# Performance work log

Measured on AMD Instinct MI355X. Metric: run time of the kernel, lower is better.

## Reference

```python
import jax, jax.numpy as jnp
import numpy as np

N, D_IN, D_OUT = 16384, 1024, 1024
E, R, TOP_K = 8, 16, 2
ALPHA = 32.0
SCALING = ALPHA / R  # standard LoRA scaling alpha/rank


def setup_inputs() -> dict:
    key = jax.random.key(0)
    k_tok, k_wb, k_a, k_b, k_g = jax.random.split(key, 5)
    tokens = jax.random.normal(k_tok, (N, D_IN), dtype=jnp.float32)
    # frozen attention projection
    W_base = jax.random.normal(k_wb, (D_IN, D_OUT), dtype=jnp.float32) * (1.0 / np.sqrt(D_IN))
    # per-expert LoRA factors
    A = jax.random.normal(k_a, (E, D_IN, R), dtype=jnp.float32) * 0.02
    B = jax.random.normal(k_b, (E, R, D_OUT), dtype=jnp.float32) * 0.02
    # router
    W_gate = jax.random.normal(k_g, (D_IN, E), dtype=jnp.float32) * (1.0 / np.sqrt(D_IN))
    return {"tokens": tokens, "W_base": W_base, "A": A, "B": B, "W_gate": W_gate}


def reference(tokens, W_base, A, B, W_gate):
    # Router: top-k gating with softmax over the selected logits
    router_logits = tokens @ W_gate                      # [N, E]
    topk_vals, selected_experts = jax.lax.top_k(router_logits, TOP_K)  # [N, K]
    expert_weights = jax.nn.softmax(topk_vals, axis=-1)  # [N, K]

    # Dense combine weights: zeros except selected experts
    gates = jnp.zeros((tokens.shape[0], E), dtype=tokens.dtype)
    gates = gates.at[jnp.arange(tokens.shape[0])[:, None], selected_experts].set(expert_weights)  # [N, E]

    # Frozen base projection
    base_out = tokens @ W_base                           # [N, D_out]

    # LoRA experts: low-rank intermediate [N, E, R] is small (rank 16)
    h = jnp.einsum('nd,edr->ner', tokens, A)             # [N, E, R]
    h = h * gates[:, :, None]                            # gate before expanding to D_out
    lora_out = jnp.einsum('ner,erm->nm', h, B)           # [N, D_out]

    out = base_out + SCALING * lora_out
    return out, router_logits, selected_experts, expert_weights
```

## Files before the change

### kernel.cpp

```cpp
#include <hip/hip_runtime.h>
#include <hip/hip_bf16.h>
#include <cstdint>
#include <cfloat>

#define NTOK 16384
#define DIN  1024
#define DOUT 1024
#define NEXP 8
#define RLORA 16
#define KTOT 1152
#define SCALE_LORA 2.0f

typedef __attribute__((ext_vector_type(8))) short bf16x8;
typedef __attribute__((ext_vector_type(4))) float f32x4;

__device__ __forceinline__ unsigned short f2bf(float f) {
  __hip_bfloat16 h = __float2bfloat16(f);
  unsigned short u;
  __builtin_memcpy(&u, &h, 2);
  return u;
}

__device__ __forceinline__ void gld_lds16(const void* g, void* l) {
  __builtin_amdgcn_global_load_lds((const __attribute__((address_space(1))) void*)g,
                                   (__attribute__((address_space(3))) void*)l,
                                   16, 0, 0);
}

__global__ __launch_bounds__(256) void k_prep(const float* __restrict__ Wb,
                                              const float* __restrict__ B,
                                              const float* __restrict__ A,
                                              const float* __restrict__ Wg,
                                              unsigned short* __restrict__ WcatT,
                                              unsigned short* __restrict__ AcatT,
                                              float* __restrict__ WgT) {
  __shared__ unsigned short Tbuf[256 * 17];
  const int bid = blockIdx.x;
  const int t = threadIdx.x;
  if (bid < 288) {
    unsigned short (*T)[66] = (unsigned short (*)[66])Tbuf;
    const int k0 = (bid % 18) * 64, j0 = (bid / 18) * 64;
#pragma unroll
    for (int p = 0; p < 4; ++p) {
      int kk = p * 16 + (t >> 4);
      int c4 = (t & 15) * 4;
      int k = k0 + kk;
      const float* src = (k < 1024) ? (Wb + (size_t)k * 1024) : (B + (size_t)(k - 1024) * 1024);
      float4 v = *(const float4*)(src + j0 + c4);
      T[kk][c4 + 0] = f2bf(v.x); T[kk][c4 + 1] = f2bf(v.y);
      T[kk][c4 + 2] = f2bf(v.z); T[kk][c4 + 3] = f2bf(v.w);
    }
    __syncthreads();
#pragma unroll
    for (int p = 0; p < 2; ++p) {
      int jj = p * 32 + (t >> 3);
      int kc = (t & 7) * 8;
      unsigned short buf[8];
#pragma unroll
      for (int i = 0; i < 8; ++i) buf[i] = T[kc + i][jj];
      uint4 u; __builtin_memcpy(&u, buf, 16);
      *(uint4*)(WcatT + (size_t)(j0 + jj) * KTOT + k0 + kc) = u;
    }
  } else if (bid < 320) {
    unsigned short (*T)[17] = (unsigned short (*)[17])Tbuf;
    const int e = (bid - 288) >> 2, d0 = ((bid - 288) & 3) * 256;
#pragma unroll
    for (int p = 0; p < 4; ++p) {
      int idx = p * 256 + t;
      int d = idx >> 2;
      int rr = (idx & 3) * 4;
      float4 v = *(const float4*)(A + (size_t)e * 16384 + (size_t)(d0 + d) * 16 + rr);
      T[d][rr + 0] = f2bf(v.x); T[d][rr + 1] = f2bf(v.y);
      T[d][rr + 2] = f2bf(v.z); T[d][rr + 3] = f2bf(v.w);
    }
    __syncthreads();
#pragma unroll
    for (int p = 0; p < 2; ++p) {
      int slot = p * 256 + t;
      int r = slot >> 5;
      int dc = (slot & 31) * 8;
      unsigned short buf[8];
#pragma unroll
      for (int i = 0; i < 8; ++i) buf[i] = T[dc + i][r];
      uint4 u; __builtin_memcpy(&u, buf, 16);
      *(uint4*)(AcatT + (size_t)(e * 16 + r) * 1024 + d0 + dc) = u;
    }
  } else {
    int d = (bid - 320) * 256 + t;
    float4 a = *(const float4*)(Wg + (size_t)d * 8);
    float4 b = *(const float4*)(Wg + (size_t)d * 8 + 4);
    WgT[0 * 1024 + d] = a.x; WgT[1 * 1024 + d] = a.y;
    WgT[2 * 1024 + d] = a.z; WgT[3 * 1024 + d] = a.w;
    WgT[4 * 1024 + d] = b.x; WgT[5 * 1024 + d] = b.y;
    WgT[6 * 1024 + d] = b.z; WgT[7 * 1024 + d] = b.w;
  }
}

__global__ __launch_bounds__(256) void k_router(const float* __restrict__ tokens,
                                                const float* __restrict__ WgT,
                                                float* __restrict__ out_logits,
                                                float* __restrict__ out_sel,
                                                float* __restrict__ out_w,
                                                unsigned short* __restrict__ Xcat,
                                                float4* __restrict__ gateinfo) {
  const int wid = threadIdx.x >> 6;
  const int lane = threadIdx.x & 63;
  const int t0 = (blockIdx.x * 4 + wid) * 2;

  float4 xa[4], xb[4];
  const float* x0 = tokens + (size_t)t0 * DIN;
  const float* x1 = x0 + DIN;
#pragma unroll
  for (int j = 0; j < 4; ++j) {
    xa[j] = *(const float4*)(x0 + j * 256 + lane * 4);
    xb[j] = *(const float4*)(x1 + j * 256 + lane * 4);
  }

#pragma unroll
  for (int tt = 0; tt < 2; ++tt) {
    unsigned short* xbp = Xcat + (size_t)(t0 + tt) * KTOT;
    const float4* xv = tt ? xb : xa;
#pragma unroll
    for (int j = 0; j < 4; ++j) {
      const float* xf = (const float*)&xv[j];
      unsigned short hb[4];
#pragma unroll
      for (int m = 0; m < 4; ++m) hb[m] = f2bf(xf[m]);
      uint2 u;
      __builtin_memcpy(&u, hb, 8);
      *(uint2*)(xbp + j * 256 + lane * 4) = u;
    }
  }

  float accA[8] = {0,0,0,0,0,0,0,0}, accB[8] = {0,0,0,0,0,0,0,0};
#pragma unroll
  for (int j = 0; j < 4; ++j) {
#pragma unroll
    for (int e = 0; e < 8; ++e) {
      float4 wv = *(const float4*)(WgT + (size_t)e * 1024 + j * 256 + lane * 4);
      accA[e] = fmaf(xa[j].x, wv.x, fmaf(xa[j].y, wv.y,
                fmaf(xa[j].z, wv.z, fmaf(xa[j].w, wv.w, accA[e]))));
      accB[e] = fmaf(xb[j].x, wv.x, fmaf(xb[j].y, wv.y,
                fmaf(xb[j].z, wv.z, fmaf(xb[j].w, wv.w, accB[e]))));
    }
  }
#pragma unroll
  for (int s = 1; s < 64; s <<= 1) {
#pragma unroll
    for (int e = 0; e < 8; ++e) {
      accA[e] += __shfl_xor(accA[e], s, 64);
      accB[e] += __shfl_xor(accB[e], s, 64);
    }
  }

#pragma unroll
  for (int tt = 0; tt < 2; ++tt) {
    const float* acc = tt ? accB : accA;
    int t = t0 + tt;
    float v0 = -FLT_MAX, v1 = -FLT_MAX;
    int i0 = -1, i1 = -1;
#pragma unroll
    for (int e = 0; e < 8; ++e) {
      float v = acc[e];
      if (v > v0) { v1 = v0; i1 = i0; v0 = v; i0 = e; }
      else if (v > v1) { v1 = v; i1 = e; }
    }
    float ex = expf(v1 - v0);
    float inv = 1.0f / (1.0f + ex);
    float w0 = inv, w1 = ex * inv;
    if (lane == 0) {
      float4* lg = (float4*)(out_logits + (size_t)t * 8);
      lg[0] = make_float4(acc[0], acc[1], acc[2], acc[3]);
      lg[1] = make_float4(acc[4], acc[5], acc[6], acc[7]);
      *(float2*)(out_sel + (size_t)t * 2) = make_float2((float)i0, (float)i1);
      *(float2*)(out_w + (size_t)t * 2) = make_float2(w0, w1);
      gateinfo[t] = make_float4((float)i0, (float)i1, w0 * SCALE_LORA, w1 * SCALE_LORA);
    }
  }
}

__global__ __launch_bounds__(256) void k_hgemm(const unsigned short* __restrict__ Xg,
                                               const unsigned short* __restrict__ Ag,
                                               const float4* __restrict__ gateinfo,
                                               unsigned short* __restrict__ Xout) {
  constexpr int BK = 64;
  __shared__ alignas(16) unsigned short As[64 * BK];
  __shared__ alignas(16) unsigned short Bs[64 * BK];
  const int tid = threadIdx.x;
  const int lane = tid & 63;
  const int wid = tid >> 6;
  const int id = blockIdx.x;
  const int xcd = id & 7, s5 = id >> 3;
  const int n0 = (s5 & 1) * 64;
  const int m0 = (xcd * 32 + (s5 >> 1)) * 64;
  const int wm = (wid >> 1) * 32, wn = (wid & 1) * 32;
  const int quad = lane >> 4, r16 = lane & 15;

  f32x4 acc[2][2] = {};

  for (int k0 = 0; k0 < 1024; k0 += BK) {
#pragma unroll
    for (int i = 0; i < 2; ++i) {
      int s = i * 256 + tid;
      int r = s >> 3, c = s & 7;
      int q = c ^ ((r >> 1) & 7);
      gld_lds16(Xg + (size_t)(m0 + r) * KTOT + k0 + q * 8, (char*)As + s * 16);
    }
#pragma unroll
    for (int i = 0; i < 2; ++i) {
      int s = i * 256 + tid;
      int r = s >> 3, c = s & 7;
      int q = c ^ ((r >> 1) & 7);
      gld_lds16(Ag + (size_t)(n0 + r) * 1024 + k0 + q * 8, (char*)Bs + s * 16);
    }
    __syncthreads();

#pragma unroll
    for (int h = 0; h < 2; ++h) {
      bf16x8 af[2], bfr[2];
#pragma unroll
      for (int mi = 0; mi < 2; ++mi) {
        int m = wm + mi * 16 + r16;
        int slot = m * 8 + ((h * 4 + quad) ^ ((m >> 1) & 7));
        af[mi] = *(const bf16x8*)((const char*)As + slot * 16);
      }
#pragma unroll
      for (int ni = 0; ni < 2; ++ni) {
        int n = wn + ni * 16 + r16;
        int slot = n * 8 + ((h * 4 + quad) ^ ((n >> 1) & 7));
        bfr[ni] = *(const bf16x8*)((const char*)Bs + slot * 16);
      }
#pragma unroll
      for (int mi = 0; mi < 2; ++mi)
#pragma unroll
        for (int ni = 0; ni < 2; ++ni)
          acc[mi][ni] = __builtin_amdgcn_mfma_f32_16x16x32_bf16(af[mi], bfr[ni], acc[mi][ni], 0, 0, 0);
    }
    __syncthreads();
  }

#pragma unroll
  for (int mi = 0; mi < 2; ++mi)
#pragma unroll
    for (int r = 0; r < 4; ++r) {
      int row = m0 + wm + mi * 16 + quad * 4 + r;
      float4 gi = gateinfo[row];
      int ie0 = (int)gi.x, ie1 = (int)gi.y;
#pragma unroll
      for (int ni = 0; ni < 2; ++ni) {
        int c = n0 + wn + ni * 16 + r16;
        int e = c >> 4;
        float h = acc[mi][ni][r];
        float v = (e == ie0) ? gi.z * h : ((e == ie1) ? gi.w * h : 0.f);
        Xout[(size_t)row * KTOT + 1024 + c] = f2bf(v);
      }
    }
}

__global__ __launch_bounds__(512, 2) void k_gemm_main(const unsigned short* __restrict__ Xg,
                                                      const unsigned short* __restrict__ Wgm,
                                                      float* __restrict__ C) {
  __shared__ alignas(16) unsigned short As[2][2][128 * 64];
  __shared__ alignas(16) unsigned short Bs[2][2][128 * 64];
  const int tid = threadIdx.x;
  const int lane = tid & 63;
  const int wid = tid >> 6;
  const int id = blockIdx.x;
  const int xcd = id & 7, loc = id >> 3;
  const int gid = xcd * 32 + loc;
  const int m0 = (gid >> 2) * 256;
  const int n0 = (gid & 3) * 256;
  const int wr64 = (wid >> 2) * 64;
  const int wc32 = (wid & 3) * 32;
  const int quad = lane >> 4, r16 = lane & 15;

  f32x4 acc[2][2][4][2] = {};
  bf16x8 af[4][2];
  bf16x8 bf_a[2][2];
  bf16x8 bf_b[2][2];

#define STAGE_A(SL, HF, KT)                                                   \
  {                                                                           \
    _Pragma("unroll")                                                         \
    for (int i_ = 0; i_ < 2; ++i_) {                                          \
      int s_ = i_ * 512 + tid;                                                \
      int r_ = s_ >> 3, c_ = s_ & 7;                                          \
      int q_ = c_ ^ ((r_ >> 1) & 7);                                          \
      gld_lds16(Xg + (size_t)(m0 + (HF) * 128 + r_) * KTOT + (KT) * 64 + q_ * 8, \
                (char*)As[SL][HF] + s_ * 16);                                 \
    }                                                                         \
  }
#define STAGE_B(SL, HF, KT)                                                   \
  {                                                                           \
    _Pragma("unroll")                                                         \
    for (int i_ = 0; i_ < 2; ++i_) {                                          \
      int s_ = i_ * 512 + tid;                                                \
      int r_ = s_ >> 3, c_ = s_ & 7;                                          \
      int q_ = c_ ^ ((r_ >> 1) & 7);                                          \
      gld_lds16(Wgm + (size_t)(n0 + (HF) * 128 + r_) * KTOT + (KT) * 64 + q_ * 8, \
                (char*)Bs[SL][HF] + s_ * 16);                                 \
    }                                                                         \
  }
#define DS_A(SL, HF)                                                          \
  {                                                                           \
    _Pragma("unroll")                                                         \
    for (int mi_ = 0; mi_ < 4; ++mi_) {                                       \
      int rh_ = wr64 + mi_ * 16 + r16;                                        \
      int sw_ = (rh_ >> 1) & 7;                                               \
      af[mi_][0] = *(const bf16x8*)((const char*)As[SL][HF] +                 \
                                    (rh_ * 8 + (quad ^ sw_)) * 16);           \
      af[mi_][1] = *(const bf16x8*)((const char*)As[SL][HF] +                 \
                                    (rh_ * 8 + ((4 + quad) ^ sw_)) * 16);     \
    }                                                                         \
  }
#define DS_B(DEST, SL, HF)                                                    \
  {                                                                           \
    _Pragma("unroll")                                                         \
    for (int ni_ = 0; ni_ < 2; ++ni_) {                                       \
      int rh_ = wc32 + ni_ * 16 + r16;                                        \
      int sw_ = (rh_ >> 1) & 7;                                               \
      DEST[ni_][0] = *(const bf16x8*)((const char*)Bs[SL][HF] +               \
                                      (rh_ * 8 + (quad ^ sw_)) * 16);         \
      DEST[ni_][1] = *(const bf16x8*)((const char*)Bs[SL][HF] +               \
                                      (rh_ * 8 + ((4 + quad) ^ sw_)) * 16);   \
    }                                                                         \
  }
#define VM(N) asm volatile("s_waitcnt vmcnt(" #N ")" ::: "memory")

#define PH(TOP, WIN, MH, NH, BF)                                              \
  {                                                                           \
    TOP;                                                                      \
    asm volatile("" ::: "memory");                                            \
    __builtin_amdgcn_s_barrier();                                             \
    asm volatile("s_waitcnt lgkmcnt(0)" ::: "memory");                        \
    __builtin_amdgcn_sched_barrier(0);                                        \
    WIN;                                                                      \
    __builtin_amdgcn_sched_barrier(0);                                        \
    __builtin_amdgcn_s_setprio(1);                                            \
    _Pragma("unroll")                                                         \
    for (int kk_ = 0; kk_ < 2; ++kk_)                                         \
      _Pragma("unroll")                                                       \
      for (int mi_ = 0; mi_ < 4; ++mi_)                                       \
        _Pragma("unroll")                                                     \
        for (int ni_ = 0; ni_ < 2; ++ni_)                                     \
          acc[MH][NH][mi_][ni_] = __builtin_amdgcn_mfma_f32_16x16x32_bf16(    \
              af[mi_][kk_], BF[ni_][kk_], acc[MH][NH][mi_][ni_], 0, 0, 0);    \
    __builtin_amdgcn_s_setprio(0);                                            \
    asm volatile("" ::: "memory");                                            \
    __builtin_amdgcn_s_barrier();                                             \
  }

  STAGE_A(0, 0, 0); STAGE_B(0, 0, 0); STAGE_B(0, 1, 0); STAGE_A(0, 1, 0);
  VM(2);
  __builtin_amdgcn_s_barrier();
  DS_B(bf_a, 0, 0);

  for (int it = 0; it < 9; ++it) {
    const int kt1 = 2 * it + 1;
    const int kt2 = (2 * it + 2 < 18) ? 2 * it + 2 : 17;
    PH(DS_A(0, 0); STAGE_A(1, 0, kt1); STAGE_B(1, 0, kt1),
       DS_B(bf_b, 0, 1), 0, 0, bf_a)
    PH(STAGE_B(1, 1, kt1); VM(6), , 0, 1, bf_b)
    PH(DS_A(0, 1), , 1, 1, bf_b)
    PH(STAGE_A(1, 1, kt1); VM(2), DS_B(bf_b, 1, 0), 1, 0, bf_a)
    PH(DS_A(1, 0); STAGE_A(0, 0, kt2); STAGE_B(0, 0, kt2),
       DS_B(bf_a, 1, 1), 0, 0, bf_b)
    PH(STAGE_B(0, 1, kt2); VM(6), , 0, 1, bf_a)
    PH(DS_A(1, 1), , 1, 1, bf_a)
    PH(STAGE_A(0, 1, kt2); VM(2), DS_B(bf_a, 0, 0), 1, 0, bf_b)
  }
  asm volatile("s_waitcnt vmcnt(0) lgkmcnt(0)" ::: "memory");
#undef PH
#undef VM
#undef DS_B
#undef DS_A
#undef STAGE_B
#undef STAGE_A

#pragma unroll
  for (int mh = 0; mh < 2; ++mh)
#pragma unroll
    for (int nh = 0; nh < 2; ++nh)
#pragma unroll
      for (int mi = 0; mi < 4; ++mi)
#pragma unroll
        for (int ni = 0; ni < 2; ++ni)
#pragma unroll
          for (int r = 0; r < 4; ++r) {
            int row = m0 + mh * 128 + wr64 + mi * 16 + quad * 4 + r;
            int cc = n0 + nh * 128 + wc32 + ni * 16 + r16;
            C[(size_t)row * 1024 + cc] = acc[mh][nh][mi][ni][r];
          }
}

extern "C" void kernel_launch(void* const* d_in, const int* in_sizes, int n_in,
                              void* d_out, int out_size, void* d_ws, size_t ws_size,
                              hipStream_t stream) {
  const float* tokens = (const float*)d_in[0];
  const float* Wb     = (const float*)d_in[1];
  const float* A      = (const float*)d_in[2];
  const float* B      = (const float*)d_in[3];
  const float* Wg     = (const float*)d_in[4];
  float* out = (float*)d_out;

  char* ws = (char*)d_ws;
  unsigned short* Xcat  = (unsigned short*)(ws);
  unsigned short* WcatT = (unsigned short*)(ws + 37748736);
  unsigned short* AcatT = (unsigned short*)(ws + 40108032);
  float4*         ginfo = (float4*)(ws + 40370176);
  float*          WgT   = (float*)(ws + 40632320);

  float* out_logits = out + (size_t)16384 * 1024;
  float* out_sel    = out_logits + (size_t)16384 * 8;
  float* out_w      = out_sel + (size_t)16384 * 2;

  k_prep<<<dim3(324), dim3(256), 0, stream>>>(Wb, B, A, Wg, WcatT, AcatT, WgT);
  k_router<<<dim3(2048), dim3(256), 0, stream>>>(tokens, WgT, out_logits, out_sel, out_w, Xcat, ginfo);
  k_hgemm<<<dim3(512), dim3(256), 0, stream>>>(Xcat, AcatT, ginfo, Xcat);
  k_gemm_main<<<dim3(256), dim3(512), 0, stream>>>(Xcat, WcatT, out);
}
```

Before: 190.0 us.

## Double-buffer LoRA h-GEMM with BK=128 and widen router bf16 stores

The LoRA intermediate GEMM now uses K tiles of 128 held in two LDS buffers, so the next tile's global-to-LDS loads are issued before the MFMAs on the current tile. One barrier per iteration replaces the previous load-sync-compute-sync pattern. The router kernel now loads 8 contiguous floats per lane and writes 16-byte bf16 stores instead of 8-byte ones. The trade-off is higher LDS use per block (64 KB), which may reduce occupancy. The h-GEMM is a small share of the total work next to the main base GEMM.

```diff
diff --git a/kernel.cpp b/kernel.cpp
--- a/kernel.cpp
+++ b/kernel.cpp
@@ -107,43 +107,47 @@
   const int lane = threadIdx.x & 63;
   const int t0 = (blockIdx.x * 4 + wid) * 2;
 
-  float4 xa[4], xb[4];
+  float4 xa[2][2], xb[2][2];
   const float* x0 = tokens + (size_t)t0 * DIN;
   const float* x1 = x0 + DIN;
 #pragma unroll
-  for (int j = 0; j < 4; ++j) {
-    xa[j] = *(const float4*)(x0 + j * 256 + lane * 4);
-    xb[j] = *(const float4*)(x1 + j * 256 + lane * 4);
-  }
+  for (int j = 0; j < 2; ++j)
+#pragma unroll
+    for (int h = 0; h < 2; ++h) {
+      xa[j][h] = *(const float4*)(x0 + j * 512 + lane * 8 + h * 4);
+      xb[j][h] = *(const float4*)(x1 + j * 512 + lane * 8 + h * 4);
+    }
 
 #pragma unroll
   for (int tt = 0; tt < 2; ++tt) {
     unsigned short* xbp = Xcat + (size_t)(t0 + tt) * KTOT;
-    const float4* xv = tt ? xb : xa;
-#pragma unroll
-    for (int j = 0; j < 4; ++j) {
-      const float* xf = (const float*)&xv[j];
-      unsigned short hb[4];
-#pragma unroll
-      for (int m = 0; m < 4; ++m) hb[m] = f2bf(xf[m]);
-      uint2 u;
-      __builtin_memcpy(&u, hb, 8);
-      *(uint2*)(xbp + j * 256 + lane * 4) = u;
+#pragma unroll
+    for (int j = 0; j < 2; ++j) {
+      const float* xf = tt ? (const float*)&xb[j][0] : (const float*)&xa[j][0];
+      unsigned short hb[8];
+#pragma unroll
+      for (int m = 0; m < 8; ++m) hb[m] = f2bf(xf[m]);
+      uint4 u;
+      __builtin_memcpy(&u, hb, 16);
+      *(uint4*)(xbp + j * 512 + lane * 8) = u;
     }
   }
 
   float accA[8] = {0,0,0,0,0,0,0,0}, accB[8] = {0,0,0,0,0,0,0,0};
 #pragma unroll
-  for (int j = 0; j < 4; ++j) {
-#pragma unroll
-    for (int e = 0; e < 8; ++e) {
-      float4 wv = *(const float4*)(WgT + (size_t)e * 1024 + j * 256 + lane * 4);
-      accA[e] = fmaf(xa[j].x, wv.x, fmaf(xa[j].y, wv.y,
-                fmaf(xa[j].z, wv.z, fmaf(xa[j].w, wv.w, accA[e]))));
-      accB[e] = fmaf(xb[j].x, wv.x, fmaf(xb[j].y, wv.y,
-                fmaf(xb[j].z, wv.z, fmaf(xb[j].w, wv.w, accB[e]))));
-    }
-  }
+  for (int j = 0; j < 2; ++j)
+#pragma unroll
+    for (int e = 0; e < 8; ++e)
+#pragma unroll
+      for (int h = 0; h < 2; ++h) {
+        float4 wv = *(const float4*)(WgT + (size_t)e * 1024 + j * 512 + lane * 8 + h * 4);
+        const float4& a4 = xa[j][h];
+        const float4& b4 = xb[j][h];
+        accA[e] = fmaf(a4.x, wv.x, fmaf(a4.y, wv.y,
+                  fmaf(a4.z, wv.z, fmaf(a4.w, wv.w, accA[e]))));
+        accB[e] = fmaf(b4.x, wv.x, fmaf(b4.y, wv.y,
+                  fmaf(b4.z, wv.z, fmaf(b4.w, wv.w, accB[e]))));
+      }
 #pragma unroll
   for (int s = 1; s < 64; s <<= 1) {
 #pragma unroll
@@ -183,9 +187,9 @@
                                                const unsigned short* __restrict__ Ag,
                                                const float4* __restrict__ gateinfo,
                                                unsigned short* __restrict__ Xout) {
-  constexpr int BK = 64;
-  __shared__ alignas(16) unsigned short As[64 * BK];
-  __shared__ alignas(16) unsigned short Bs[64 * BK];
+  constexpr int BK = 128;
+  __shared__ alignas(16) unsigned short As[2][64 * BK];
+  __shared__ alignas(16) unsigned short Bs[2][64 * BK];
   const int tid = threadIdx.x;
   const int lane = tid & 63;
   const int wid = tid >> 6;
@@ -198,46 +202,66 @@
 
   f32x4 acc[2][2] = {};
 
-  for (int k0 = 0; k0 < 1024; k0 += BK) {
-#pragma unroll
-    for (int i = 0; i < 2; ++i) {
-      int s = i * 256 + tid;
-      int r = s >> 3, c = s & 7;
-      int q = c ^ ((r >> 1) & 7);
-      gld_lds16(Xg + (size_t)(m0 + r) * KTOT + k0 + q * 8, (char*)As + s * 16);
-    }
-#pragma unroll
-    for (int i = 0; i < 2; ++i) {
-      int s = i * 256 + tid;
-      int r = s >> 3, c = s & 7;
-      int q = c ^ ((r >> 1) & 7);
-      gld_lds16(Ag + (size_t)(n0 + r) * 1024 + k0 + q * 8, (char*)Bs + s * 16);
-    }
-    __syncthreads();
-
-#pragma unroll
-    for (int h = 0; h < 2; ++h) {
-      bf16x8 af[2], bfr[2];
-#pragma unroll
-      for (int mi = 0; mi < 2; ++mi) {
-        int m = wm + mi * 16 + r16;
-        int slot = m * 8 + ((h * 4 + quad) ^ ((m >> 1) & 7));
-        af[mi] = *(const bf16x8*)((const char*)As + slot * 16);
-      }
-#pragma unroll
-      for (int ni = 0; ni < 2; ++ni) {
-        int n = wn + ni * 16 + r16;
-        int slot = n * 8 + ((h * 4 + quad) ^ ((n >> 1) & 7));
-        bfr[ni] = *(const bf16x8*)((const char*)Bs + slot * 16);
-      }
+#define HSTAGE(d, k0s)                                                        \
+  {                                                                           \
+    _Pragma("unroll")                                                         \
+    for (int i_ = 0; i_ < 4; ++i_) {                                          \
+      int s_ = i_ * 256 + tid;                                                \
+      int r_ = s_ >> 4, c_ = s_ & 15;                                         \
+      int q_ = c_ ^ ((r_ >> 1) & 7);                                          \
+      gld_lds16(Xg + (size_t)(m0 + r_) * KTOT + (k0s) + q_ * 8,               \
+                (char*)As[d] + s_ * 16);                                      \
+    }                                                                         \
+    _Pragma("unroll")                                                         \
+    for (int i_ = 0; i_ < 4; ++i_) {                                          \
+      int s_ = i_ * 256 + tid;                                                \
+      int r_ = s_ >> 4, c_ = s_ & 15;                                         \
+      int q_ = c_ ^ ((r_ >> 1) & 7);                                          \
+      gld_lds16(Ag + (size_t)(n0 + r_) * 1024 + (k0s) + q_ * 8,               \
+                (char*)Bs[d] + s_ * 16);                                      \
+    }                                                                         \
+  }
+
+  HSTAGE(0, 0);
+  asm volatile("s_waitcnt vmcnt(0)" ::: "memory");
+  __builtin_amdgcn_s_barrier();
+
+  int cur = 0;
+  for (int t = 0; t < 8; ++t) {
+    if (t < 7) HSTAGE(cur ^ 1, (t + 1) * BK);
+
+    bf16x8 af[2][4], bfr[2][4];
+#pragma unroll
+    for (int mi = 0; mi < 2; ++mi) {
+      int m = wm + mi * 16 + r16;
+      int sw = (m >> 1) & 7;
+#pragma unroll
+      for (int h = 0; h < 4; ++h)
+        af[mi][h] = *(const bf16x8*)((const char*)As[cur] +
+                                     (m * 16 + ((h * 4 + quad) ^ sw)) * 16);
+    }
+#pragma unroll
+    for (int ni = 0; ni < 2; ++ni) {
+      int n = wn + ni * 16 + r16;
+      int sw = (n >> 1) & 7;
+#pragma unroll
+      for (int h = 0; h < 4; ++h)
+        bfr[ni][h] = *(const bf16x8*)((const char*)Bs[cur] +
+                                      (n * 16 + ((h * 4 + quad) ^ sw)) * 16);
+    }
+#pragma unroll
+    for (int h = 0; h < 4; ++h)
 #pragma unroll
       for (int mi = 0; mi < 2; ++mi)
 #pragma unroll
         for (int ni = 0; ni < 2; ++ni)
-          acc[mi][ni] = __builtin_amdgcn_mfma_f32_16x16x32_bf16(af[mi], bfr[ni], acc[mi][ni], 0, 0, 0);
-    }
-    __syncthreads();
-  }
+          acc[mi][ni] = __builtin_amdgcn_mfma_f32_16x16x32_bf16(af[mi][h], bfr[ni][h], acc[mi][ni], 0, 0, 0);
+
+    asm volatile("s_waitcnt vmcnt(0)" ::: "memory");
+    __builtin_amdgcn_s_barrier();
+    cur ^= 1;
+  }
+#undef HSTAGE
 
 #pragma unroll
   for (int mi = 0; mi < 2; ++mi)
```

Result: slower. 194.6 us (+2.4%).

## Fuse router and LoRA down-projection into one kernel with LDS-resident token tile

Applied to the files above, without the earlier changes.

Merges the router kernel and the low-rank h-GEMM into a single kernel. Each block converts 32 token rows to bf16, keeps them in swizzled shared memory and computes gating, then runs the rank GEMM against double-buffered A tiles without re-reading X from global memory. Gate info stays in shared memory instead of a global buffer. The cost is 64KB+ of LDS per block, which lowers occupancy, and only 512 blocks that each process 32 rows serially in the router phase.

```diff
diff --git a/kernel.cpp b/kernel.cpp
--- a/kernel.cpp
+++ b/kernel.cpp
@@ -96,164 +96,157 @@
   }
 }
 
-__global__ __launch_bounds__(256) void k_router(const float* __restrict__ tokens,
-                                                const float* __restrict__ WgT,
-                                                float* __restrict__ out_logits,
-                                                float* __restrict__ out_sel,
-                                                float* __restrict__ out_w,
-                                                unsigned short* __restrict__ Xcat,
-                                                float4* __restrict__ gateinfo) {
-  const int wid = threadIdx.x >> 6;
-  const int lane = threadIdx.x & 63;
-  const int t0 = (blockIdx.x * 4 + wid) * 2;
-
-  float4 xa[4], xb[4];
-  const float* x0 = tokens + (size_t)t0 * DIN;
-  const float* x1 = x0 + DIN;
-#pragma unroll
-  for (int j = 0; j < 4; ++j) {
-    xa[j] = *(const float4*)(x0 + j * 256 + lane * 4);
-    xb[j] = *(const float4*)(x1 + j * 256 + lane * 4);
-  }
-
-#pragma unroll
-  for (int tt = 0; tt < 2; ++tt) {
-    unsigned short* xbp = Xcat + (size_t)(t0 + tt) * KTOT;
-    const float4* xv = tt ? xb : xa;
-#pragma unroll
-    for (int j = 0; j < 4; ++j) {
-      const float* xf = (const float*)&xv[j];
-      unsigned short hb[4];
-#pragma unroll
-      for (int m = 0; m < 4; ++m) hb[m] = f2bf(xf[m]);
-      uint2 u;
-      __builtin_memcpy(&u, hb, 8);
-      *(uint2*)(xbp + j * 256 + lane * 4) = u;
-    }
-  }
-
-  float accA[8] = {0,0,0,0,0,0,0,0}, accB[8] = {0,0,0,0,0,0,0,0};
-#pragma unroll
-  for (int j = 0; j < 4; ++j) {
-#pragma unroll
-    for (int e = 0; e < 8; ++e) {
-      float4 wv = *(const float4*)(WgT + (size_t)e * 1024 + j * 256 + lane * 4);
-      accA[e] = fmaf(xa[j].x, wv.x, fmaf(xa[j].y, wv.y,
-                fmaf(xa[j].z, wv.z, fmaf(xa[j].w, wv.w, accA[e]))));
-      accB[e] = fmaf(xb[j].x, wv.x, fmaf(xb[j].y, wv.y,
-                fmaf(xb[j].z, wv.z, fmaf(xb[j].w, wv.w, accB[e]))));
-    }
-  }
-#pragma unroll
-  for (int s = 1; s < 64; s <<= 1) {
-#pragma unroll
-    for (int e = 0; e < 8; ++e) {
-      accA[e] += __shfl_xor(accA[e], s, 64);
-      accB[e] += __shfl_xor(accB[e], s, 64);
-    }
-  }
-
-#pragma unroll
-  for (int tt = 0; tt < 2; ++tt) {
-    const float* acc = tt ? accB : accA;
-    int t = t0 + tt;
-    float v0 = -FLT_MAX, v1 = -FLT_MAX;
-    int i0 = -1, i1 = -1;
-#pragma unroll
-    for (int e = 0; e < 8; ++e) {
-      float v = acc[e];
-      if (v > v0) { v1 = v0; i1 = i0; v0 = v; i0 = e; }
-      else if (v > v1) { v1 = v; i1 = e; }
-    }
-    float ex = expf(v1 - v0);
-    float inv = 1.0f / (1.0f + ex);
-    float w0 = inv, w1 = ex * inv;
-    if (lane == 0) {
-      float4* lg = (float4*)(out_logits + (size_t)t * 8);
-      lg[0] = make_float4(acc[0], acc[1], acc[2], acc[3]);
-      lg[1] = make_float4(acc[4], acc[5], acc[6], acc[7]);
-      *(float2*)(out_sel + (size_t)t * 2) = make_float2((float)i0, (float)i1);
-      *(float2*)(out_w + (size_t)t * 2) = make_float2(w0, w1);
-      gateinfo[t] = make_float4((float)i0, (float)i1, w0 * SCALE_LORA, w1 * SCALE_LORA);
-    }
-  }
-}
-
-__global__ __launch_bounds__(256) void k_hgemm(const unsigned short* __restrict__ Xg,
-                                               const unsigned short* __restrict__ Ag,
-                                               const float4* __restrict__ gateinfo,
-                                               unsigned short* __restrict__ Xout) {
-  constexpr int BK = 64;
-  __shared__ alignas(16) unsigned short As[64 * BK];
-  __shared__ alignas(16) unsigned short Bs[64 * BK];
+__global__ __launch_bounds__(256) void k_rh(const float* __restrict__ tokens,
+                                            const float* __restrict__ WgT,
+                                            const unsigned short* __restrict__ Ag,
+                                            float* __restrict__ out_logits,
+                                            float* __restrict__ out_sel,
+                                            float* __restrict__ out_w,
+                                            unsigned short* __restrict__ Xcat) {
+  __shared__ alignas(16) unsigned short Xl[32 * 1024];
+  __shared__ alignas(16) unsigned short Bsl[2][128 * 64];
+  __shared__ float4 gtab[32];
   const int tid = threadIdx.x;
   const int lane = tid & 63;
   const int wid = tid >> 6;
-  const int id = blockIdx.x;
-  const int xcd = id & 7, s5 = id >> 3;
-  const int n0 = (s5 & 1) * 64;
-  const int m0 = (xcd * 32 + (s5 >> 1)) * 64;
-  const int wm = (wid >> 1) * 32, wn = (wid & 1) * 32;
+  const int id = (int)blockIdx.x;
+  const int gid = (id & 7) * 64 + (id >> 3);
+  const int m0 = gid * 32;
+
+  for (int p = 0; p < 4; ++p) {
+    const int r0 = wid * 8 + p * 2;
+    const float* x0 = tokens + (size_t)(m0 + r0) * DIN;
+    const float* x1 = x0 + DIN;
+    float4 xa[4], xb[4];
+#pragma unroll
+    for (int j = 0; j < 4; ++j) {
+      xa[j] = *(const float4*)(x0 + j * 256 + lane * 4);
+      xb[j] = *(const float4*)(x1 + j * 256 + lane * 4);
+    }
+#pragma unroll
+    for (int tt = 0; tt < 2; ++tt) {
+      const int rr = r0 + tt;
+      unsigned short* xbp = Xcat + (size_t)(m0 + rr) * KTOT;
+      const float4* xv = tt ? xb : xa;
+#pragma unroll
+      for (int j = 0; j < 4; ++j) {
+        const float* xf = (const float*)&xv[j];
+        unsigned short hb[4];
+#pragma unroll
+        for (int m = 0; m < 4; ++m) hb[m] = f2bf(xf[m]);
+        uint2 u;
+        __builtin_memcpy(&u, hb, 8);
+        int d = j * 256 + lane * 4;
+        *(uint2*)(xbp + d) = u;
+        int cj = d >> 3;
+        char* dst = (char*)Xl + ((size_t)rr * 128 + (cj ^ (rr & 7))) * 16 + (d & 7) * 2;
+        *(uint2*)dst = u;
+      }
+    }
+    float accA[8] = {0,0,0,0,0,0,0,0}, accB[8] = {0,0,0,0,0,0,0,0};
+#pragma unroll
+    for (int j = 0; j < 4; ++j) {
+#pragma unroll
+      for (int e = 0; e < 8; ++e) {
+        float4 wv = *(const float4*)(WgT + (size_t)e * 1024 + j * 256 + lane * 4);
+        accA[e] = fmaf(xa[j].x, wv.x, fmaf(xa[j].y, wv.y,
+                  fmaf(xa[j].z, wv.z, fmaf(xa[j].w, wv.w, accA[e]))));
+        accB[e] = fmaf(xb[j].x, wv.x, fmaf(xb[j].y, wv.y,
+                  fmaf(xb[j].z, wv.z, fmaf(xb[j].w, wv.w, accB[e]))));
+      }
+    }
+#pragma unroll
+    for (int s = 1; s < 64; s <<= 1) {
+#pragma unroll
+      for (int e = 0; e < 8; ++e) {
+        accA[e] += __shfl_xor(accA[e], s, 64);
+        accB[e] += __shfl_xor(accB[e], s, 64);
+      }
+    }
+#pragma unroll
+    for (int tt = 0; tt < 2; ++tt) {
+      const float* acc = tt ? accB : accA;
+      int rl = r0 + tt;
+      int t = m0 + rl;
+      float v0 = -FLT_MAX, v1 = -FLT_MAX;
+      int i0 = -1, i1 = -1;
+#pragma unroll
+      for (int e = 0; e < 8; ++e) {
+        float v = acc[e];
+        if (v > v0) { v1 = v0; i1 = i0; v0 = v; i0 = e; }
+        else if (v > v1) { v1 = v; i1 = e; }
+      }
+      float ex = expf(v1 - v0);
+      float inv = 1.0f / (1.0f + ex);
+      float w0 = inv, w1 = ex * inv;
+      if (lane == 0) {
+        float4* lg = (float4*)(out_logits + (size_t)t * 8);
+        lg[0] = make_float4(acc[0], acc[1], acc[2], acc[3]);
+        lg[1] = make_float4(acc[4], acc[5], acc[6], acc[7]);
+        *(float2*)(out_sel + (size_t)t * 2) = make_float2((float)i0, (float)i1);
+        *(float2*)(out_w + (size_t)t * 2) = make_float2(w0, w1);
+        gtab[rl] = make_float4((float)i0, (float)i1, w0 * SCALE_LORA, w1 * SCALE_LORA);
+      }
+    }
+  }
+
+#define BSTAGE(d, kt)                                                         \
+  {                                                                           \
+    _Pragma("unroll")                                                         \
+    for (int i_ = 0; i_ < 4; ++i_) {                                          \
+      int s_ = i_ * 256 + tid;                                                \
+      int r_ = s_ >> 3, c_ = s_ & 7;                                          \
+      int q_ = c_ ^ ((r_ >> 1) & 7);                                          \
+      gld_lds16(Ag + (size_t)r_ * 1024 + (kt) * 64 + q_ * 8,                  \
+                (char*)Bsl[d] + s_ * 16);                                     \
+    }                                                                         \
+  }
+
+  BSTAGE(0, 0);
+  __syncthreads();
+
+  const int wm = (wid >> 1) * 16, wn = (wid & 1) * 64;
   const int quad = lane >> 4, r16 = lane & 15;
-
-  f32x4 acc[2][2] = {};
-
-  for (int k0 = 0; k0 < 1024; k0 += BK) {
-#pragma unroll
-    for (int i = 0; i < 2; ++i) {
-      int s = i * 256 + tid;
-      int r = s >> 3, c = s & 7;
-      int q = c ^ ((r >> 1) & 7);
-      gld_lds16(Xg + (size_t)(m0 + r) * KTOT + k0 + q * 8, (char*)As + s * 16);
-    }
-#pragma unroll
-    for (int i = 0; i < 2; ++i) {
-      int s = i * 256 + tid;
-      int r = s >> 3, c = s & 7;
-      int q = c ^ ((r >> 1) & 7);
-      gld_lds16(Ag + (size_t)(n0 + r) * 1024 + k0 + q * 8, (char*)Bs + s * 16);
-    }
+  f32x4 acc[4] = {};
+  int cur = 0;
+  for (int t = 0; t < 16; ++t) {
+    if (t < 15) BSTAGE(cur ^ 1, t + 1);
+    bf16x8 af[2], bfr[4][2];
+    const int m = wm + r16;
+#pragma unroll
+    for (int kk = 0; kk < 2; ++kk)
+      af[kk] = *(const bf16x8*)((const char*)Xl +
+                ((size_t)m * 128 + ((t * 8 + kk * 4 + quad) ^ (m & 7))) * 16);
+#pragma unroll
+    for (int ni = 0; ni < 4; ++ni) {
+      int n = wn + ni * 16 + r16;
+      int sw = (n >> 1) & 7;
+#pragma unroll
+      for (int kk = 0; kk < 2; ++kk)
+        bfr[ni][kk] = *(const bf16x8*)((const char*)Bsl[cur] +
+                      ((size_t)n * 8 + ((kk * 4 + quad) ^ sw)) * 16);
+    }
+#pragma unroll
+    for (int kk = 0; kk < 2; ++kk)
+#pragma unroll
+      for (int ni = 0; ni < 4; ++ni)
+        acc[ni] = __builtin_amdgcn_mfma_f32_16x16x32_bf16(af[kk], bfr[ni][kk], acc[ni], 0, 0, 0);
     __syncthreads();
-
-#pragma unroll
-    for (int h = 0; h < 2; ++h) {
-      bf16x8 af[2], bfr[2];
-#pragma unroll
-      for (int mi = 0; mi < 2; ++mi) {
-        int m = wm + mi * 16 + r16;
-        int slot = m * 8 + ((h * 4 + quad) ^ ((m >> 1) & 7));
-        af[mi] = *(const bf16x8*)((const char*)As + slot * 16);
-      }
-#pragma unroll
-      for (int ni = 0; ni < 2; ++ni) {
-        int n = wn + ni * 16 + r16;
-        int slot = n * 8 + ((h * 4 + quad) ^ ((n >> 1) & 7));
-        bfr[ni] = *(const bf16x8*)((const char*)Bs + slot * 16);
-      }
-#pragma unroll
-      for (int mi = 0; mi < 2; ++mi)
-#pragma unroll
-        for (int ni = 0; ni < 2; ++ni)
-          acc[mi][ni] = __builtin_amdgcn_mfma_f32_16x16x32_bf16(af[mi], bfr[ni], acc[mi][ni], 0, 0, 0);
-    }
-    __syncthreads();
-  }
-
-#pragma unroll
-  for (int mi = 0; mi < 2; ++mi)
+    cur ^= 1;
+  }
+#undef BSTAGE
+
+#pragma unroll
+  for (int ni = 0; ni < 4; ++ni)
 #pragma unroll
     for (int r = 0; r < 4; ++r) {
-      int row = m0 + wm + mi * 16 + quad * 4 + r;
-      float4 gi = gateinfo[row];
-      int ie0 = (int)gi.x, ie1 = (int)gi.y;
-#pragma unroll
-      for (int ni = 0; ni < 2; ++ni) {
-        int c = n0 + wn + ni * 16 + r16;
-        int e = c >> 4;
-        float h = acc[mi][ni][r];
-        float v = (e == ie0) ? gi.z * h : ((e == ie1) ? gi.w * h : 0.f);
-        Xout[(size_t)row * KTOT + 1024 + c] = f2bf(v);
-      }
+      int rl = wm + quad * 4 + r;
+      float4 gi = gtab[rl];
+      int col = wn + ni * 16 + r16;
+      int e = col >> 4;
+      float h = acc[ni][r];
+      float v = (e == (int)gi.x) ? gi.z * h : ((e == (int)gi.y) ? gi.w * h : 0.f);
+      Xcat[(size_t)(m0 + rl) * KTOT + 1024 + col] = f2bf(v);
     }
 }
 
@@ -407,7 +400,6 @@
   unsigned short* Xcat  = (unsigned short*)(ws);
   unsigned short* WcatT = (unsigned short*)(ws + 37748736);
   unsigned short* AcatT = (unsigned short*)(ws + 40108032);
-  float4*         ginfo = (float4*)(ws + 40370176);
   float*          WgT   = (float*)(ws + 40632320);
 
   float* out_logits = out + (size_t)16384 * 1024;
@@ -415,7 +407,6 @@
   float* out_w      = out_sel + (size_t)16384 * 2;
 
   k_prep<<<dim3(324), dim3(256), 0, stream>>>(Wb, B, A, Wg, WcatT, AcatT, WgT);
-  k_router<<<dim3(2048), dim3(256), 0, stream>>>(tokens, WgT, out_logits, out_sel, out_w, Xcat, ginfo);
-  k_hgemm<<<dim3(512), dim3(256), 0, stream>>>(Xcat, AcatT, ginfo, Xcat);
+  k_rh<<<dim3(512), dim3(256), 0, stream>>>(tokens, WgT, AcatT, out_logits, out_sel, out_w, Xcat);
   k_gemm_main<<<dim3(256), dim3(512), 0, stream>>>(Xcat, WcatT, out);
 }
```

Result: slower. 205.0 us (+7.9%).
